# Performance work log

Hardware: AMD Instinct MI355X
Metric: run time of the kernel (lower is better)

## Reference

```python
import jax, jax.numpy as jnp
from jax import lax
import numpy as np

PROB = 0.4
SNR_LO, SNR_HI = 0.5, 3.0
BF_LO, BF_HI = 0.1, 0.5
MAX_CH = 0.5
FS = 256
B, C, T = 64, 64, 15360


def setup_inputs() -> dict:
    key = jax.random.key(0)
    ks = jax.random.split(key, 8)
    return {
        "x": jax.random.normal(ks[0], (B, C, T), dtype=jnp.float32),
        "noise": jax.random.normal(ks[1], (B, C, T), dtype=jnp.float32),
        "apply_u": jax.random.uniform(ks[2], (B,), dtype=jnp.float32),
        "frac_u": jax.random.uniform(ks[3], (B,), dtype=jnp.float32),
        "ch_u": jax.random.uniform(ks[4], (B, C), dtype=jnp.float32),
        "burst_u": jax.random.uniform(ks[5], (B,), dtype=jnp.float32),
        "start_u": jax.random.uniform(ks[6], (B,), dtype=jnp.float32),
        "snr_u": jax.random.uniform(ks[7], (B,), dtype=jnp.float32),
    }


def _emg_inject(x, noise, apply_u, frac_u, ch_u, burst_u, start_u, snr_u):
    b, c, t = x.shape
    # --- highpass: noise - moving average (torch conv1d, zero pad) ---
    k = max(3, FS // 10)
    if k % 2 == 0:
        k += 1  # -> 25
    ker = jnp.ones((1, 1, k), noise.dtype) / k
    low = lax.conv_general_dilated(
        noise.reshape(b * c, 1, t), ker, (1,), [(k // 2, k // 2)],
        dimension_numbers=("NCH", "OIH", "NCH")).reshape(b, c, t)
    emg = noise - low  # (B,C,T)

    # --- per-sample burst mask with linear edge ramps ---
    blen = lax.stop_gradient(jnp.floor(t * (BF_LO + burst_u * (BF_HI - BF_LO))).astype(jnp.int32))  # (B,)
    start = lax.stop_gradient(jnp.floor(start_u * jnp.maximum(t - blen, 1).astype(jnp.float32)).astype(jnp.int32))
    elen = jnp.minimum(25, blen // 4)

    tt = jnp.arange(t, dtype=jnp.float32)[None, :]          # (1,T)
    sf = start.astype(jnp.float32)[:, None]                  # (B,1)
    bf = blen.astype(jnp.float32)[:, None]
    ef = elen.astype(jnp.float32)[:, None]
    end = sf + bf
    denom = jnp.maximum(ef - 1.0, 1.0)
    in_burst = (tt >= sf) & (tt < end)
    up = (tt - sf) / denom                                   # linspace(0,1,elen)
    down = (end - 1.0 - tt) / denom                          # linspace(1,0,elen)
    ramped = jnp.where(tt < sf + ef, up, jnp.where(tt >= end - ef, down, 1.0))
    mask = jnp.where(in_burst, jnp.where(ef > 1.0, ramped, 1.0), 0.0)  # (B,T)

    # --- random affected-channel subset (randperm[:n_affected]) ---
    n_aff = jnp.maximum(1, jnp.floor(c * frac_u * MAX_CH).astype(jnp.int32))  # (B,)
    ch_rank = jnp.argsort(jnp.argsort(ch_u, axis=1), axis=1)                  # (B,C)
    ch_mask = (ch_rank < n_aff[:, None]).astype(x.dtype)                      # (B,C)

    emg_b = emg * mask[:, None, :]
    sig_p = jnp.sqrt(jnp.mean(x * x, axis=-1, keepdims=True)) + 1e-8          # (B,C,1)
    noi_p = jnp.sqrt(jnp.mean(emg_b * emg_b, axis=-1, keepdims=True)) + 1e-8
    snr = (SNR_LO + snr_u * (SNR_HI - SNR_LO))[:, None, None]
    scaled = emg_b * (sig_p / (noi_p * snr))

    sel = (apply_u <= PROB).astype(x.dtype)[:, None, None] * ch_mask[:, :, None]
    return x + sel * scaled


def reference(x, noise, apply_u, frac_u, ch_u, burst_u, start_u, snr_u):
    return _emg_inject(x, noise, apply_u, frac_u, ch_u, burst_u, start_u, snr_u)
```

## Files before the change

kernel.cpp:

```cpp
#include <hip/hip_runtime.h>
#include <math.h>

constexpr int T_LEN = 15360;
constexpr int B_DIM = 64;
constexpr int C_DIM = 64;
constexpr int NTHR  = 256;
constexpr int KHALF = 12;
constexpr int SEG    = 12;
constexpr int CH     = T_LEN / SEG;
constexpr int EPT    = CH / NTHR;
constexpr int F4SEG  = CH / 4;

__device__ __forceinline__ int compute_affected(const float* __restrict__ ch_u,
                                                const float* __restrict__ frac_u,
                                                const float* __restrict__ apply_u,
                                                int b, int c, int tid, int* s_aff)
{
    if (tid < 64) {
        const float myv = ch_u[(size_t)b * C_DIM + c];
        const float v   = ch_u[(size_t)b * C_DIM + tid];
        const bool pred = (v < myv) || (v == myv && tid < c);
        unsigned long long m = __ballot(pred);
        if (tid == 0) {
            int rank  = (int)__popcll(m);
            int n_aff = (int)floorf(((float)C_DIM * frac_u[b]) * 0.5f);
            if (n_aff < 1) n_aff = 1;
            *s_aff = (apply_u[b] <= 0.4f && rank < n_aff) ? 1 : 0;
        }
    }
    __syncthreads();
    return *s_aff;
}

struct BurstParams {
    float sf, endf, ef, inv_denom, head_end, tail_beg;
};

__device__ __forceinline__ BurstParams burst_params(const float* __restrict__ burst_u,
                                                    const float* __restrict__ start_u,
                                                    int b)
{
    const float bu   = burst_u[b];
    const float bfr  = 0.1f + bu * 0.4f;
    const int   blen = (int)floorf((float)T_LEN * bfr);
    int tmb = T_LEN - blen; if (tmb < 1) tmb = 1;
    const int   start = (int)floorf(start_u[b] * (float)tmb);
    const int   elen  = min(25, blen / 4);
    BurstParams p;
    p.sf   = (float)start;
    p.endf = p.sf + (float)blen;
    p.ef   = (float)elen;
    const float denom = fmaxf(p.ef - 1.0f, 1.0f);
    p.inv_denom = 1.0f / denom;
    p.head_end  = p.sf + p.ef;
    p.tail_beg  = p.endf - p.ef;
    return p;
}

__device__ __forceinline__ void stage_noise(const float* __restrict__ nrow, int g0,
                                            float* s_buf, int tid)
{
    const float4* nsrc = (const float4*)(nrow + g0);
    float4* sb4 = (float4*)(s_buf + KHALF);
    #pragma unroll
    for (int it = 0; it < 2; ++it) {
        int q = tid + it * NTHR;
        if (q < F4SEG) sb4[q] = nsrc[q];
    }
    if (tid < KHALF) {
        int gl = g0 - KHALF + tid;
        s_buf[tid] = (gl >= 0) ? nrow[gl] : 0.f;
        int gr = g0 + CH + tid;
        s_buf[KHALF + CH + tid] = (gr < T_LEN) ? nrow[gr] : 0.f;
    }
}

__global__ __launch_bounds__(NTHR, 8)
void emg_stats_kernel(const float* __restrict__ x,
                      const float* __restrict__ noise,
                      const float* __restrict__ apply_u,
                      const float* __restrict__ frac_u,
                      const float* __restrict__ ch_u,
                      const float* __restrict__ burst_u,
                      const float* __restrict__ start_u,
                      float* __restrict__ ws)
{
    const int row = blockIdx.x;
    const int seg = blockIdx.y;
    const int b   = row >> 6;
    const int c   = row & 63;
    const int tid = threadIdx.x;

    __shared__ int   s_aff;
    __shared__ float s_red[8];
    __shared__ __align__(16) float s_buf[CH + 2 * KHALF + 1];

    if (!compute_affected(ch_u, frac_u, apply_u, b, c, tid, &s_aff)) return;

    const BurstParams p = burst_params(burst_u, start_u, b);
    const float inv_k = 1.0f / 25.0f;
    const int g0 = seg * CH;

    const float4* x4 = (const float4*)(x + (size_t)row * T_LEN + g0);
    float sumx2 = 0.f;
    #pragma unroll
    for (int it = 0; it < 2; ++it) {
        int q = tid + it * NTHR;
        if (q < F4SEG) {
            float4 xv = x4[q];
            sumx2 += xv.x * xv.x + xv.y * xv.y + xv.z * xv.z + xv.w * xv.w;
        }
    }

    const float* nrow = noise + (size_t)row * T_LEN;
    stage_noise(nrow, g0, s_buf, tid);
    __syncthreads();

    const int l0 = KHALF + tid * EPT;
    float w = 0.f;
    #pragma unroll
    for (int d = -KHALF; d <= KHALF; ++d) w += s_buf[l0 + d];
    float sume2 = 0.f;
    #pragma unroll
    for (int j = 0; j < EPT; ++j) {
        const float nv  = s_buf[l0 + j];
        const float emg = nv - w * inv_k;
        const float tt  = (float)(g0 + tid * EPT + j);
        const bool  inb = (tt >= p.sf) && (tt < p.endf);
        float ramped;
        if (tt < p.head_end)       ramped = (tt - p.sf) * p.inv_denom;
        else if (tt >= p.tail_beg) ramped = (p.endf - 1.0f - tt) * p.inv_denom;
        else                       ramped = 1.0f;
        const float m  = inb ? ((p.ef > 1.0f) ? ramped : 1.0f) : 0.0f;
        const float eb = emg * m;
        sume2 += eb * eb;
        if (j < EPT - 1)
            w += s_buf[l0 + j + KHALF + 1] - s_buf[l0 + j - KHALF];
    }

    float v1 = sumx2, v2 = sume2;
    #pragma unroll
    for (int off = 32; off > 0; off >>= 1) {
        v1 += __shfl_down(v1, off, 64);
        v2 += __shfl_down(v2, off, 64);
    }
    const int wave = tid >> 6;
    if ((tid & 63) == 0) { s_red[wave] = v1; s_red[wave + 4] = v2; }
    __syncthreads();
    if (tid == 0) {
        float sx = s_red[0] + s_red[1] + s_red[2] + s_red[3];
        float se = s_red[4] + s_red[5] + s_red[6] + s_red[7];
        float* wdst = ws + ((size_t)row * SEG + seg) * 2;
        wdst[0] = sx;
        wdst[1] = se;
    }
}

__global__ __launch_bounds__(NTHR, 8)
void emg_apply_kernel(const float* __restrict__ x,
                      const float* __restrict__ noise,
                      const float* __restrict__ apply_u,
                      const float* __restrict__ frac_u,
                      const float* __restrict__ ch_u,
                      const float* __restrict__ burst_u,
                      const float* __restrict__ start_u,
                      const float* __restrict__ snr_u,
                      const float* __restrict__ ws,
                      float* __restrict__ out)
{
    const int row = blockIdx.x;
    const int seg = blockIdx.y;
    const int b   = row >> 6;
    const int c   = row & 63;
    const int tid = threadIdx.x;

    __shared__ int s_aff;
    __shared__ __align__(16) float s_buf[CH + 2 * KHALF + 1];

    const int g0 = seg * CH;
    const float4* x4 = (const float4*)(x   + (size_t)row * T_LEN + g0);
    float4*       o4 = (float4*)      (out + (size_t)row * T_LEN + g0);

    if (!compute_affected(ch_u, frac_u, apply_u, b, c, tid, &s_aff)) {
        #pragma unroll
        for (int it = 0; it < 2; ++it) {
            int q = tid + it * NTHR;
            if (q < F4SEG) o4[q] = x4[q];
        }
        return;
    }

    const float* wrow = ws + (size_t)row * SEG * 2;
    float sx = 0.f, se = 0.f;
    #pragma unroll
    for (int s = 0; s < SEG; ++s) { sx += wrow[2 * s]; se += wrow[2 * s + 1]; }

    const float sig_p = sqrtf(sx / (float)T_LEN) + 1e-8f;
    const float noi_p = sqrtf(se / (float)T_LEN) + 1e-8f;
    const float snr   = 0.5f + snr_u[b] * 2.5f;
    const float coef  = sig_p / (noi_p * snr);

    const BurstParams p = burst_params(burst_u, start_u, b);
    const float inv_k = 1.0f / 25.0f;

    const float* nrow = noise + (size_t)row * T_LEN;
    stage_noise(nrow, g0, s_buf, tid);
    __syncthreads();

    const int l0 = KHALF + tid * EPT;
    float w = 0.f;
    #pragma unroll
    for (int d = -KHALF; d <= KHALF; ++d) w += s_buf[l0 + d];
    float e[EPT];
    #pragma unroll
    for (int j = 0; j < EPT; ++j) {
        const float nv  = s_buf[l0 + j];
        const float emg = nv - w * inv_k;
        const float tt  = (float)(g0 + tid * EPT + j);
        const bool  inb = (tt >= p.sf) && (tt < p.endf);
        float ramped;
        if (tt < p.head_end)       ramped = (tt - p.sf) * p.inv_denom;
        else if (tt >= p.tail_beg) ramped = (p.endf - 1.0f - tt) * p.inv_denom;
        else                       ramped = 1.0f;
        const float m  = inb ? ((p.ef > 1.0f) ? ramped : 1.0f) : 0.0f;
        e[j] = emg * m;
        if (j < EPT - 1)
            w += s_buf[l0 + j + KHALF + 1] - s_buf[l0 + j - KHALF];
    }
    __syncthreads();

    #pragma unroll
    for (int j = 0; j < EPT; ++j) s_buf[l0 + j] = e[j];
    __syncthreads();

    const float4* sb4 = (const float4*)(s_buf + KHALF);
    #pragma unroll
    for (int it = 0; it < 2; ++it) {
        int q = tid + it * NTHR;
        if (q < F4SEG) {
            float4 ev = sb4[q];
            float4 xv = x4[q];
            float4 ov;
            ov.x = xv.x + coef * ev.x;
            ov.y = xv.y + coef * ev.y;
            ov.z = xv.z + coef * ev.z;
            ov.w = xv.w + coef * ev.w;
            o4[q] = ov;
        }
    }
}

extern "C" void kernel_launch(void* const* d_in, const int* in_sizes, int n_in,
                              void* d_out, int out_size, void* d_ws, size_t ws_size,
                              hipStream_t stream) {
    const float* x       = (const float*)d_in[0];
    const float* noise   = (const float*)d_in[1];
    const float* apply_u = (const float*)d_in[2];
    const float* frac_u  = (const float*)d_in[3];
    const float* ch_u    = (const float*)d_in[4];
    const float* burst_u = (const float*)d_in[5];
    const float* start_u = (const float*)d_in[6];
    const float* snr_u   = (const float*)d_in[7];
    float* out = (float*)d_out;
    float* ws  = (float*)d_ws;

    dim3 grid(B_DIM * C_DIM, SEG);
    dim3 block(NTHR);
    emg_stats_kernel<<<grid, block, 0, stream>>>(
        x, noise, apply_u, frac_u, ch_u, burst_u, start_u, ws);
    emg_apply_kernel<<<grid, block, 0, stream>>>(
        x, noise, apply_u, frac_u, ch_u, burst_u, start_u, snr_u, ws, out);
}
```

Baseline: 134.9 us.

## Fuse stats and apply kernels with a last-block-per-row completion counter

Replaces the separate statistics and apply kernels with one kernel. Each segment block writes partial sums and bumps a per-row atomic counter, and the last-arriving block reduces them and applies the scaled EMG to the whole row. This removes one kernel launch and the global barrier between the passes. In exchange, a single block serially processes all 12 chunks of each affected row, which can create a tail and reduces parallelism in the apply phase. It also adds a memset for the counters.

```diff
diff --git a/kernel.cpp b/kernel.cpp
--- a/kernel.cpp
+++ b/kernel.cpp
@@ -75,143 +75,14 @@
     }
 }
 
-__global__ __launch_bounds__(NTHR, 8)
-void emg_stats_kernel(const float* __restrict__ x,
-                      const float* __restrict__ noise,
-                      const float* __restrict__ apply_u,
-                      const float* __restrict__ frac_u,
-                      const float* __restrict__ ch_u,
-                      const float* __restrict__ burst_u,
-                      const float* __restrict__ start_u,
-                      float* __restrict__ ws)
-{
-    const int row = blockIdx.x;
-    const int seg = blockIdx.y;
-    const int b   = row >> 6;
-    const int c   = row & 63;
-    const int tid = threadIdx.x;
-
-    __shared__ int   s_aff;
-    __shared__ float s_red[8];
-    __shared__ __align__(16) float s_buf[CH + 2 * KHALF + 1];
-
-    if (!compute_affected(ch_u, frac_u, apply_u, b, c, tid, &s_aff)) return;
-
-    const BurstParams p = burst_params(burst_u, start_u, b);
+__device__ __forceinline__ void compute_emgb(const float* s_buf, int g0, int tid,
+                                             const BurstParams& p, float* e)
+{
     const float inv_k = 1.0f / 25.0f;
-    const int g0 = seg * CH;
-
-    const float4* x4 = (const float4*)(x + (size_t)row * T_LEN + g0);
-    float sumx2 = 0.f;
-    #pragma unroll
-    for (int it = 0; it < 2; ++it) {
-        int q = tid + it * NTHR;
-        if (q < F4SEG) {
-            float4 xv = x4[q];
-            sumx2 += xv.x * xv.x + xv.y * xv.y + xv.z * xv.z + xv.w * xv.w;
-        }
-    }
-
-    const float* nrow = noise + (size_t)row * T_LEN;
-    stage_noise(nrow, g0, s_buf, tid);
-    __syncthreads();
-
     const int l0 = KHALF + tid * EPT;
     float w = 0.f;
     #pragma unroll
     for (int d = -KHALF; d <= KHALF; ++d) w += s_buf[l0 + d];
-    float sume2 = 0.f;
-    #pragma unroll
-    for (int j = 0; j < EPT; ++j) {
-        const float nv  = s_buf[l0 + j];
-        const float emg = nv - w * inv_k;
-        const float tt  = (float)(g0 + tid * EPT + j);
-        const bool  inb = (tt >= p.sf) && (tt < p.endf);
-        float ramped;
-        if (tt < p.head_end)       ramped = (tt - p.sf) * p.inv_denom;
-        else if (tt >= p.tail_beg) ramped = (p.endf - 1.0f - tt) * p.inv_denom;
-        else                       ramped = 1.0f;
-        const float m  = inb ? ((p.ef > 1.0f) ? ramped : 1.0f) : 0.0f;
-        const float eb = emg * m;
-        sume2 += eb * eb;
-        if (j < EPT - 1)
-            w += s_buf[l0 + j + KHALF + 1] - s_buf[l0 + j - KHALF];
-    }
-
-    float v1 = sumx2, v2 = sume2;
-    #pragma unroll
-    for (int off = 32; off > 0; off >>= 1) {
-        v1 += __shfl_down(v1, off, 64);
-        v2 += __shfl_down(v2, off, 64);
-    }
-    const int wave = tid >> 6;
-    if ((tid & 63) == 0) { s_red[wave] = v1; s_red[wave + 4] = v2; }
-    __syncthreads();
-    if (tid == 0) {
-        float sx = s_red[0] + s_red[1] + s_red[2] + s_red[3];
-        float se = s_red[4] + s_red[5] + s_red[6] + s_red[7];
-        float* wdst = ws + ((size_t)row * SEG + seg) * 2;
-        wdst[0] = sx;
-        wdst[1] = se;
-    }
-}
-
-__global__ __launch_bounds__(NTHR, 8)
-void emg_apply_kernel(const float* __restrict__ x,
-                      const float* __restrict__ noise,
-                      const float* __restrict__ apply_u,
-                      const float* __restrict__ frac_u,
-                      const float* __restrict__ ch_u,
-                      const float* __restrict__ burst_u,
-                      const float* __restrict__ start_u,
-                      const float* __restrict__ snr_u,
-                      const float* __restrict__ ws,
-                      float* __restrict__ out)
-{
-    const int row = blockIdx.x;
-    const int seg = blockIdx.y;
-    const int b   = row >> 6;
-    const int c   = row & 63;
-    const int tid = threadIdx.x;
-
-    __shared__ int s_aff;
-    __shared__ __align__(16) float s_buf[CH + 2 * KHALF + 1];
-
-    const int g0 = seg * CH;
-    const float4* x4 = (const float4*)(x   + (size_t)row * T_LEN + g0);
-    float4*       o4 = (float4*)      (out + (size_t)row * T_LEN + g0);
-
-    if (!compute_affected(ch_u, frac_u, apply_u, b, c, tid, &s_aff)) {
-        #pragma unroll
-        for (int it = 0; it < 2; ++it) {
-            int q = tid + it * NTHR;
-            if (q < F4SEG) o4[q] = x4[q];
-        }
-        return;
-    }
-
-    const float* wrow = ws + (size_t)row * SEG * 2;
-    float sx = 0.f, se = 0.f;
-    #pragma unroll
-    for (int s = 0; s < SEG; ++s) { sx += wrow[2 * s]; se += wrow[2 * s + 1]; }
-
-    const float sig_p = sqrtf(sx / (float)T_LEN) + 1e-8f;
-    const float noi_p = sqrtf(se / (float)T_LEN) + 1e-8f;
-    const float snr   = 0.5f + snr_u[b] * 2.5f;
-    const float coef  = sig_p / (noi_p * snr);
-
-    const BurstParams p = burst_params(burst_u, start_u, b);
-    const float inv_k = 1.0f / 25.0f;
-
-    const float* nrow = noise + (size_t)row * T_LEN;
-    stage_noise(nrow, g0, s_buf, tid);
-    __syncthreads();
-
-    const int l0 = KHALF + tid * EPT;
-    float w = 0.f;
-    #pragma unroll
-    for (int d = -KHALF; d <= KHALF; ++d) w += s_buf[l0 + d];
-    float e[EPT];
     #pragma unroll
     for (int j = 0; j < EPT; ++j) {
         const float nv  = s_buf[l0 + j];
@@ -227,25 +98,137 @@
         if (j < EPT - 1)
             w += s_buf[l0 + j + KHALF + 1] - s_buf[l0 + j - KHALF];
     }
-    __syncthreads();
-
-    #pragma unroll
-    for (int j = 0; j < EPT; ++j) s_buf[l0 + j] = e[j];
-    __syncthreads();
-
-    const float4* sb4 = (const float4*)(s_buf + KHALF);
+}
+
+__global__ __launch_bounds__(NTHR, 6)
+void emg_fused_kernel(const float* __restrict__ x,
+                      const float* __restrict__ noise,
+                      const float* __restrict__ apply_u,
+                      const float* __restrict__ frac_u,
+                      const float* __restrict__ ch_u,
+                      const float* __restrict__ burst_u,
+                      const float* __restrict__ start_u,
+                      const float* __restrict__ snr_u,
+                      int*   __restrict__ counters,
+                      float* __restrict__ partials,
+                      float* __restrict__ out)
+{
+    const int idx = blockIdx.x;
+    const int row = idx / SEG;
+    const int seg = idx - row * SEG;
+    const int b   = row >> 6;
+    const int c   = row & 63;
+    const int tid = threadIdx.x;
+
+    __shared__ int   s_flag;
+    __shared__ float s_red[8];
+    __shared__ __align__(16) float s_buf[CH + 2 * KHALF + 1];
+
+    const int g0 = seg * CH;
+    const float*  xrow = x   + (size_t)row * T_LEN;
+    float*        orow = out + (size_t)row * T_LEN;
+    const float4* x4   = (const float4*)(xrow + g0);
+
+    if (!compute_affected(ch_u, frac_u, apply_u, b, c, tid, &s_flag)) {
+        float4* o4 = (float4*)(orow + g0);
+        #pragma unroll
+        for (int it = 0; it < 2; ++it) {
+            int q = tid + it * NTHR;
+            if (q < F4SEG) o4[q] = x4[q];
+        }
+        return;
+    }
+
+    const BurstParams p = burst_params(burst_u, start_u, b);
+    const float* nrow = noise + (size_t)row * T_LEN;
+
+    float sumx2 = 0.f;
     #pragma unroll
     for (int it = 0; it < 2; ++it) {
         int q = tid + it * NTHR;
         if (q < F4SEG) {
-            float4 ev = sb4[q];
             float4 xv = x4[q];
-            float4 ov;
-            ov.x = xv.x + coef * ev.x;
-            ov.y = xv.y + coef * ev.y;
-            ov.z = xv.z + coef * ev.z;
-            ov.w = xv.w + coef * ev.w;
-            o4[q] = ov;
+            sumx2 += xv.x * xv.x + xv.y * xv.y + xv.z * xv.z + xv.w * xv.w;
+        }
+    }
+
+    stage_noise(nrow, g0, s_buf, tid);
+    __syncthreads();
+
+    float e[EPT];
+    compute_emgb(s_buf, g0, tid, p, e);
+    float sume2 = 0.f;
+    #pragma unroll
+    for (int j = 0; j < EPT; ++j) sume2 += e[j] * e[j];
+
+    float v1 = sumx2, v2 = sume2;
+    #pragma unroll
+    for (int off = 32; off > 0; off >>= 1) {
+        v1 += __shfl_down(v1, off, 64);
+        v2 += __shfl_down(v2, off, 64);
+    }
+    const int wave = tid >> 6;
+    if ((tid & 63) == 0) { s_red[wave] = v1; s_red[wave + 4] = v2; }
+    __syncthreads();
+
+    if (tid == 0) {
+        float sx = s_red[0] + s_red[1] + s_red[2] + s_red[3];
+        float se = s_red[4] + s_red[5] + s_red[6] + s_red[7];
+        float* wdst = partials + ((size_t)row * SEG + seg) * 2;
+        wdst[0] = sx;
+        wdst[1] = se;
+        __threadfence();
+        int old = atomicAdd(&counters[row], 1);
+        s_flag = (old == SEG - 1) ? 1 : 0;
+    }
+    __syncthreads();
+    if (!s_flag) return;
+
+    if (tid == 0) {
+        __threadfence();
+        const float* wrow = partials + (size_t)row * SEG * 2;
+        float sx = 0.f, se = 0.f;
+        #pragma unroll
+        for (int s = 0; s < SEG; ++s) { sx += wrow[2 * s]; se += wrow[2 * s + 1]; }
+        const float sig_p = sqrtf(sx / (float)T_LEN) + 1e-8f;
+        const float noi_p = sqrtf(se / (float)T_LEN) + 1e-8f;
+        const float snr   = 0.5f + snr_u[b] * 2.5f;
+        s_red[0] = sig_p / (noi_p * snr);
+    }
+    __syncthreads();
+    const float coef = s_red[0];
+
+    for (int ck = 0; ck < SEG; ++ck) {
+        const int cg0 = ck * CH;
+        __syncthreads();
+        stage_noise(nrow, cg0, s_buf, tid);
+        __syncthreads();
+
+        float ec[EPT];
+        compute_emgb(s_buf, cg0, tid, p, ec);
+        __syncthreads();
+
+        const int l0 = KHALF + tid * EPT;
+        #pragma unroll
+        for (int j = 0; j < EPT; ++j) s_buf[l0 + j] = ec[j];
+        __syncthreads();
+
+        const float4* sb4  = (const float4*)(s_buf + KHALF);
+        const float4* xsrc = (const float4*)(xrow + cg0);
+        float4*       odst = (float4*)(orow + cg0);
+        #pragma unroll
+        for (int it = 0; it < 2; ++it) {
+            int q = tid + it * NTHR;
+            if (q < F4SEG) {
+                float4 ev = sb4[q];
+                float4 xv = xsrc[q];
+                float4 ov;
+                ov.x = xv.x + coef * ev.x;
+                ov.y = xv.y + coef * ev.y;
+                ov.z = xv.z + coef * ev.z;
+                ov.w = xv.w + coef * ev.w;
+                odst[q] = ov;
+            }
         }
     }
 }
@@ -262,12 +245,15 @@
     const float* start_u = (const float*)d_in[6];
     const float* snr_u   = (const float*)d_in[7];
     float* out = (float*)d_out;
-    float* ws  = (float*)d_ws;
-
-    dim3 grid(B_DIM * C_DIM, SEG);
+
+    int*   counters = (int*)d_ws;
+    float* partials = (float*)((char*)d_ws + 16 * 1024);
+
+    hipMemsetAsync(counters, 0, B_DIM * C_DIM * sizeof(int), stream);
+
+    dim3 grid(B_DIM * C_DIM * SEG);
     dim3 block(NTHR);
-    emg_stats_kernel<<<grid, block, 0, stream>>>(
-        x, noise, apply_u, frac_u, ch_u, burst_u, start_u, ws);
-    emg_apply_kernel<<<grid, block, 0, stream>>>(
-        x, noise, apply_u, frac_u, ch_u, burst_u, start_u, snr_u, ws, out);
-}
+    emg_fused_kernel<<<grid, block, 0, stream>>>(
+        x, noise, apply_u, frac_u, ch_u, burst_u, start_u, snr_u,
+        counters, partials, out);
+}
```

Result: slower. 503.3 us (+273.2%).
